# Kernel tuning notes

Measured on AMD Instinct MI355X. Metric: run time of the kernel, lower is better.

The kernel has to match this reference:

```python
import jax, jax.numpy as jnp
import numpy as np

DIM, HEADS, WS, SHIFT, HID = 256, 8, 7, 3, 1024
N = WS * WS

def _rel_index():
    coords = np.stack(np.meshgrid(np.arange(WS), np.arange(WS), indexing='ij')).reshape(2, -1)
    rel = (coords[:, :, None] - coords[:, None, :]).transpose(1, 2, 0)
    rel[:, :, 0] += WS - 1
    rel[:, :, 1] += WS - 1
    rel[:, :, 0] *= 2 * WS - 1
    return rel.sum(-1)  # [N, N] int

def _attn_mask(hp, wp):
    img = np.zeros((hp, wp))
    slices = (slice(0, -WS), slice(-WS, -SHIFT), slice(-SHIFT, None))
    cnt = 0
    for hs in slices:
        for ws_ in slices:
            img[hs, ws_] = cnt
            cnt += 1
    mw = img.reshape(hp // WS, WS, wp // WS, WS).transpose(0, 2, 1, 3).reshape(-1, N)
    am = mw[:, None, :] - mw[:, :, None]  # [nw, N, N]
    return np.where(am != 0, -100.0, 0.0).astype(np.float32)

def _ln(t, g, b):
    mu = t.mean(-1, keepdims=True)
    var = ((t - mu) ** 2).mean(-1, keepdims=True)
    return (t - mu) / jnp.sqrt(var + 1e-5) * g + b

def setup_inputs() -> dict:
    key = jax.random.key(0)
    ks = jax.random.split(key, 16)
    b, h, w = 16, 112, 112
    p = lambda k, shape: jax.random.normal(k, shape, dtype=jnp.float32) * 0.02
    return {
        'x': jax.random.normal(ks[0], (b, h * w, DIM), dtype=jnp.float32),
        'norm1_w': jnp.ones((DIM,), jnp.float32), 'norm1_b': jnp.zeros((DIM,), jnp.float32),
        'qkv_w': p(ks[1], (DIM, 3 * DIM)), 'qkv_b': jnp.zeros((3 * DIM,), jnp.float32),
        'proj_w': p(ks[2], (DIM, DIM)), 'proj_b': jnp.zeros((DIM,), jnp.float32),
        'bias_table': p(ks[3], ((2 * WS - 1) * (2 * WS - 1), HEADS)),
        'norm2_w': jnp.ones((DIM,), jnp.float32), 'norm2_b': jnp.zeros((DIM,), jnp.float32),
        'fc1_w': p(ks[4], (DIM, HID)), 'fc1_b': jnp.zeros((HID,), jnp.float32),
        'fc2_w': p(ks[5], (HID, DIM)), 'fc2_b': jnp.zeros((DIM,), jnp.float32),
        'h': h, 'w': w,
    }

def reference(x, norm1_w, norm1_b, qkv_w, qkv_b, proj_w, proj_b, bias_table,
              norm2_w, norm2_b, fc1_w, fc1_b, fc2_w, fc2_b, h, w):
    b, l, c = x.shape
    hd = c // HEADS
    shortcut = x
    xn = _ln(x, norm1_w, norm1_b).reshape(b, h, w, c)
    pad_b, pad_r = (-h) % WS, (-w) % WS
    if pad_b or pad_r:
        xn = jnp.pad(xn, ((0, 0), (0, pad_b), (0, pad_r), (0, 0)))
    hp, wp = h + pad_b, w + pad_r
    xs = jnp.roll(xn, (-SHIFT, -SHIFT), (1, 2))
    # window partition -> [B_, N, c]
    win = xs.reshape(b, hp // WS, WS, wp // WS, WS, c).transpose(0, 1, 3, 2, 4, 5).reshape(-1, N, c)
    qkv = (win @ qkv_w + qkv_b).reshape(-1, N, 3, HEADS, hd).transpose(2, 0, 3, 1, 4)
    q, k, v = qkv[0] * (hd ** -0.5), qkv[1], qkv[2]
    attn = jnp.einsum('bhnd,bhmd->bhnm', q, k)  # [B_, H, N, N]
    rpb = bias_table[jnp.asarray(_rel_index().reshape(-1))].reshape(N, N, HEADS).transpose(2, 0, 1)
    attn = attn + rpb[None]
    mask = jnp.asarray(_attn_mask(hp, wp))  # [nw, N, N]
    nw = mask.shape[0]
    attn = (attn.reshape(b, nw, HEADS, N, N) + mask[None, :, None]).reshape(-1, HEADS, N, N)
    attn = jax.nn.softmax(attn, axis=-1)
    out = jnp.einsum('bhnm,bhmd->bhnd', attn, v).transpose(0, 2, 1, 3).reshape(-1, N, c)
    out = out @ proj_w + proj_b
    # window reverse
    out = out.reshape(b, hp // WS, wp // WS, WS, WS, c).transpose(0, 1, 3, 2, 4, 5).reshape(b, hp, wp, c)
    out = jnp.roll(out, (SHIFT, SHIFT), (1, 2))[:, :h, :w].reshape(b, h * w, c)
    x = shortcut + out
    x = x + (jax.nn.gelu(_ln(x, norm2_w, norm2_b) @ fc1_w + fc1_b, approximate=False) @ fc2_w + fc2_b)
    return x
```

## Files before the change

kernel.cpp:

```cpp
#include <hip/hip_runtime.h>
#include <stdint.h>
#include <math.h>

#define DIMC   256
#define NHEADS 8
#define WSZ    7
#define NTOK   49
#define HIDN   1024
#define IMGS   112
#define BATCH  16
#define NWIN   4096
#define MTOT   200704

using frag_ab = __attribute__((ext_vector_type(8))) short;
using frag_cd = __attribute__((ext_vector_type(4))) float;

__device__ __forceinline__ float b2f(ushort u) {
    union { float f; uint32_t i; } c; c.i = ((uint32_t)u) << 16; return c.f;
}
__device__ __forceinline__ ushort f2b(float f) {
    union { float f; uint32_t i; } c; c.f = f;
    uint32_t r = c.i + 0x7fffu + ((c.i >> 16) & 1u);
    return (ushort)(r >> 16);
}

__device__ __forceinline__ void gld16(const ushort* g, ushort* l) {
    __builtin_amdgcn_global_load_lds(
        (const __attribute__((address_space(1))) void*)g,
        (__attribute__((address_space(3))) void*)l, 16, 0, 0);
}

__global__ void detect_kernel(const uint32_t* __restrict__ w, int* __restrict__ flag) {
    if (threadIdx.x == 0 && blockIdx.x == 0)
        *flag = (w[0] == 0x3F800000u) ? 1 : 0;
}

__global__ void cvt_kernel(const void* __restrict__ src, ushort* __restrict__ dst,
                           int n, const int* __restrict__ dflag) {
    int i = blockIdx.x * 256 + threadIdx.x;
    if (i < n)
        dst[i] = (*dflag) ? f2b(((const float*)src)[i]) : ((const ushort*)src)[i];
}

__global__ void transpose_cvt(const void* __restrict__ src, ushort* __restrict__ dst,
                              int K, int N, const int* __restrict__ dflag) {
    int idx = blockIdx.x * 256 + threadIdx.x;
    if (idx < K * N) {
        int k = idx / N, n = idx - k * N;
        ushort v = (*dflag) ? f2b(((const float*)src)[idx]) : ((const ushort*)src)[idx];
        dst[n * K + k] = v;
    }
}

__global__ __launch_bounds__(256)
void zero_vpad(ushort* __restrict__ vt) {
    int idx = blockIdx.x * 256 + threadIdx.x;
    float4 z = {0.f, 0.f, 0.f, 0.f};
    *(float4*)(vt + ((size_t)(idx >> 1) << 6) + 48 + (idx & 1) * 8) = z;
}

template <bool REMAP>
__global__ __launch_bounds__(256)
void ln_kernel(const void* __restrict__ xin, const ushort* __restrict__ g,
               const ushort* __restrict__ bt, ushort* __restrict__ out,
               const int* __restrict__ dflag) {
    int gw = (blockIdx.x * 256 + threadIdx.x) >> 6;
    int lane = threadIdx.x & 63;
    if (gw >= MTOT) return;
    float v0, v1, v2, v3;
    if constexpr (REMAP) {
        if (*dflag) {
            float4 xv = *(const float4*)((const float*)xin + (size_t)gw * DIMC + lane * 4);
            v0 = xv.x; v1 = xv.y; v2 = xv.z; v3 = xv.w;
        } else {
            ushort4 xv = *(const ushort4*)((const ushort*)xin + (size_t)gw * DIMC + lane * 4);
            v0 = b2f(xv.x); v1 = b2f(xv.y); v2 = b2f(xv.z); v3 = b2f(xv.w);
        }
    } else {
        ushort4 xv = *(const ushort4*)((const ushort*)xin + (size_t)gw * DIMC + lane * 4);
        v0 = b2f(xv.x); v1 = b2f(xv.y); v2 = b2f(xv.z); v3 = b2f(xv.w);
    }
    float s = v0 + v1 + v2 + v3;
#pragma unroll
    for (int off = 32; off; off >>= 1) s += __shfl_xor(s, off);
    float mean = s * (1.f / 256.f);
    float d0 = v0 - mean, d1 = v1 - mean, d2 = v2 - mean, d3 = v3 - mean;
    float q = d0 * d0 + d1 * d1 + d2 * d2 + d3 * d3;
#pragma unroll
    for (int off = 32; off; off >>= 1) q += __shfl_xor(q, off);
    float inv = rsqrtf(q * (1.f / 256.f) + 1e-5f);
    ushort4 gv = *(const ushort4*)(g + lane * 4);
    ushort4 bv = *(const ushort4*)(bt + lane * 4);
    ushort4 o;
    o.x = f2b(d0 * inv * b2f(gv.x) + b2f(bv.x));
    o.y = f2b(d1 * inv * b2f(gv.y) + b2f(bv.y));
    o.z = f2b(d2 * inv * b2f(gv.z) + b2f(bv.z));
    o.w = f2b(d3 * inv * b2f(gv.w) + b2f(bv.w));
    size_t orow;
    if constexpr (REMAP) {
        int b = gw / 12544, sres = gw - b * 12544;
        int row = sres / IMGS, col = sres - row * IMGS;
        int r = row - 3; if (r < 0) r += IMGS;
        int c = col - 3; if (c < 0) c += IMGS;
        int wh = r / WSZ, tr = r - wh * WSZ;
        int ww = c / WSZ, tc = c - ww * WSZ;
        orow = (size_t)(((b * 16 + wh) * 16 + ww)) * NTOK + (tr * WSZ + tc);
    } else {
        orow = gw;
    }
    *(ushort4*)(out + orow * DIMC + lane * 4) = o;
}

template <int MODE>
__global__ __launch_bounds__(256)
void gemm_bt(const ushort* __restrict__ A, const ushort* __restrict__ Bt,
             const ushort* __restrict__ bias, void* __restrict__ outv,
             const void* __restrict__ add, int M, int N, int K,
             const int* __restrict__ dflag) {
    __shared__ __align__(16) ushort As[2][128 * 32];
    __shared__ __align__(16) ushort Bs[2][128 * 32];
    const int t = threadIdx.x;
    const int lane = t & 63, wave = t >> 6;
    const int wr = (wave >> 1) * 64, wc = (wave & 1) * 64;
    const int lrow = lane & 15, lq8 = (lane >> 4) * 8;
    const int bm = blockIdx.y * 128, bn = blockIdx.x * 128;
    const int arow = t >> 2, acol = (t & 3) * 8;

    int isf32 = 0;
    if constexpr (MODE == 1) isf32 = *dflag;

    frag_cd acc[4][4];
#pragma unroll
    for (int i = 0; i < 4; i++)
#pragma unroll
        for (int j = 0; j < 4; j++) acc[i][j] = (frag_cd){0.f, 0.f, 0.f, 0.f};

    const ushort* Ag0 = A + (size_t)(bm + arow) * K + acol;
    const ushort* Ag1 = Ag0 + (size_t)64 * K;
    const ushort* Bg0 = Bt + (size_t)(bn + arow) * K + acol;
    const ushort* Bg1 = Bg0 + (size_t)64 * K;
    const int lofs0 = arow * 32 + acol;
    const int lofs1 = (arow + 64) * 32 + acol;

    gld16(Ag0, &As[0][lofs0]);
    gld16(Ag1, &As[0][lofs1]);
    gld16(Bg0, &Bs[0][lofs0]);
    gld16(Bg1, &Bs[0][lofs1]);
    __syncthreads();

    int cur = 0;
    for (int kk = 0; kk < K; kk += 32) {
        const int nxt = cur ^ 1;
        if (kk + 32 < K) {
            gld16(Ag0 + kk + 32, &As[nxt][lofs0]);
            gld16(Ag1 + kk + 32, &As[nxt][lofs1]);
            gld16(Bg0 + kk + 32, &Bs[nxt][lofs0]);
            gld16(Bg1 + kk + 32, &Bs[nxt][lofs1]);
        }
        frag_ab af[4], bfr[4];
#pragma unroll
        for (int i = 0; i < 4; i++)
            af[i] = *(const frag_ab*)&As[cur][(wr + i * 16 + lrow) * 32 + lq8];
#pragma unroll
        for (int j = 0; j < 4; j++)
            bfr[j] = *(const frag_ab*)&Bs[cur][(wc + j * 16 + lrow) * 32 + lq8];
#pragma unroll
        for (int i = 0; i < 4; i++)
#pragma unroll
            for (int j = 0; j < 4; j++)
                acc[i][j] = __builtin_amdgcn_mfma_f32_16x16x32_bf16(
                    af[i], bfr[j], acc[i][j], 0, 0, 0);
        __syncthreads();
        cur = nxt;
    }

    ushort* out = (ushort*)outv;
    float*  outf = (float*)outv;

#pragma unroll
    for (int i = 0; i < 4; i++) {
#pragma unroll
        for (int rg = 0; rg < 4; rg++) {
            const int gm = bm + wr + i * 16 + (lane >> 4) * 4 + rg;
            int win = 0, tok = 0;
            size_t rowbase = 0;
            if constexpr (MODE == 0) {
                win = gm / 49; tok = gm - win * 49;
            } else if constexpr (MODE == 1) {
                win = gm / 49; tok = gm - win * 49;
                int b = win >> 8, wh = (win >> 4) & 15, ww = win & 15;
                int tr = tok / 7, tc = tok - tr * 7;
                int r = wh * 7 + tr + 3; if (r >= IMGS) r -= IMGS;
                int c = ww * 7 + tc + 3; if (c >= IMGS) c -= IMGS;
                rowbase = ((size_t)b * 12544 + r * IMGS + c) * DIMC;
            } else {
                rowbase = (size_t)gm * N;
            }
#pragma unroll
            for (int j = 0; j < 4; j++) {
                const int gn = bn + wc + j * 16 + lrow;
                float v = acc[i][j][rg] + b2f(bias[gn]);
                if constexpr (MODE == 0) {
                    int part = gn >> 8, hd = (gn >> 5) & 7, dd = gn & 31;
                    if (part == 0) v *= 0.17677669529663687f;
                    if (part == 2) {
                        out[(size_t)2 * MTOT * DIMC +
                            (((size_t)win * NHEADS + hd) * 32 + dd) * 64 + tok] = f2b(v);
                    } else {
                        out[(size_t)part * ((size_t)MTOT * DIMC) +
                            (((size_t)win * NHEADS + hd) * NTOK + tok) * 32 + dd] = f2b(v);
                    }
                } else if constexpr (MODE == 1) {
                    float r = isf32 ? ((const float*)add)[rowbase + gn]
                                    : b2f(((const ushort*)add)[rowbase + gn]);
                    v += r;
                    out[rowbase + gn] = f2b(v);
                } else if constexpr (MODE == 2) {
                    v = 0.5f * v * (1.f + erff(v * 0.70710678118654752f));
                    out[rowbase + gn] = f2b(v);
                } else {
                    v += b2f(((const ushort*)add)[rowbase + gn]);
                    outf[rowbase + gn] = v;
                }
            }
        }
    }
}

__global__ __launch_bounds__(256)
void attn_kernel(const ushort* __restrict__ qb, const ushort* __restrict__ kb,
                 const ushort* __restrict__ vtb, const ushort* __restrict__ btab,
                 ushort* __restrict__ out) {
    __shared__ __align__(16) ushort Pl[4][2][16][72];
    __shared__ float bbs[4][172];
    const int t = threadIdx.x;
    const int wv = t >> 6, l = t & 63;
    const int lo = l & 15, hi = l >> 4;
    const int gw = blockIdx.x * 4 + wv;
    const int win = gw >> 3, hd = gw & 7;
    const int wh = (win >> 4) & 15, ww = win & 15;

    for (int idx = l; idx < 169; idx += 64)
        bbs[wv][idx] = b2f(btab[idx * NHEADS + hd]);

    const ushort* qp = qb  + (size_t)gw * (NTOK * 32);
    const ushort* kp = kb  + (size_t)gw * (NTOK * 32);
    const ushort* vp = vtb + (size_t)gw * (32 * 64);

    frag_ab af[4], bfr[4];
#pragma unroll
    for (int i = 0; i < 4; i++) {
        af[i]  = *(const frag_ab*)(qp + (i * 16 + lo) * 32 + hi * 8);
        bfr[i] = *(const frag_ab*)(kp + (i * 16 + lo) * 32 + hi * 8);
    }
    frag_ab vf[2][2];
#pragma unroll
    for (int j = 0; j < 2; j++)
#pragma unroll
        for (int kk = 0; kk < 2; kk++)
            vf[j][kk] = *(const frag_ab*)(vp + (j * 16 + lo) * 64 + kk * 32 + hi * 8);

    frag_cd S[4][4];
#pragma unroll
    for (int i = 0; i < 4; i++)
#pragma unroll
        for (int j = 0; j < 4; j++) S[i][j] = (frag_cd){0.f, 0.f, 0.f, 0.f};
#pragma unroll
    for (int i = 0; i < 4; i++)
#pragma unroll
        for (int j = 0; j < 4; j++)
            S[i][j] = __builtin_amdgcn_mfma_f32_16x16x32_bf16(af[i], bfr[j], S[i][j], 0, 0, 0);

    int cy[4], cx[4], rvj[4], rhj[4];
#pragma unroll
    for (int j = 0; j < 4; j++) {
        int c = j * 16 + lo;
        int y = (c * 9363) >> 16;
        cy[j] = y; cx[j] = c - y * 7;
        rvj[j] = (wh < 15) ? 0 : ((cy[j] < 4) ? 1 : 2);
        rhj[j] = (ww < 15) ? 0 : ((cx[j] < 4) ? 1 : 2);
    }

    frag_cd o[4][2];
#pragma unroll
    for (int i = 0; i < 4; i++)
#pragma unroll
        for (int j = 0; j < 2; j++) o[i][j] = (frag_cd){0.f, 0.f, 0.f, 0.f};

#pragma unroll
    for (int i = 0; i < 4; i++) {
        const int cur = i & 1;
#pragma unroll
        for (int rg = 0; rg < 4; rg++) {
            int r = i * 16 + hi * 4 + rg;
            int rr = (r < NTOK) ? r : 0;
            int yi = (rr * 9363) >> 16, xi = rr - yi * 7;
            int rvi = (wh < 15) ? 0 : ((yi < 4) ? 1 : 2);
            int rhi = (ww < 15) ? 0 : ((xi < 4) ? 1 : 2);
            float xs[4];
#pragma unroll
            for (int j = 0; j < 4; j++) {
                bool valid = (j < 3) | (lo == 0);
                float v = S[i][j][rg]
                        + bbs[wv][(yi - cy[j] + 6) * 13 + (xi - cx[j] + 6)];
                v = (rvi != rvj[j] || rhi != rhj[j]) ? v - 100.f : v;
                xs[j] = valid ? v : -1e30f;
            }
            float m = fmaxf(fmaxf(xs[0], xs[1]), fmaxf(xs[2], xs[3]));
#pragma unroll
            for (int off = 8; off; off >>= 1) m = fmaxf(m, __shfl_xor(m, off));
            float e0 = __expf(xs[0] - m);
            float e1 = __expf(xs[1] - m);
            float e2 = __expf(xs[2] - m);
            float e3 = __expf(xs[3] - m);
            float sum = e0 + e1 + e2 + e3;
#pragma unroll
            for (int off = 8; off; off >>= 1) sum += __shfl_xor(sum, off);
            float inv = 1.f / sum;
            int rl = hi * 4 + rg;
            int sw = ((rl >> 3) & 1) << 4;
            ushort* prow = &Pl[wv][cur][rl][0];
            prow[(lo +  0) ^ sw] = f2b(e0 * inv);
            prow[(lo + 16) ^ sw] = f2b(e1 * inv);
            prow[(lo + 32) ^ sw] = f2b(e2 * inv);
            prow[(lo + 48) ^ sw] = f2b(e3 * inv);
        }
        int swr = ((lo >> 3) & 1) << 4;
        frag_ab pa0 = *(const frag_ab*)&Pl[wv][cur][lo][(      hi * 8) ^ swr];
        frag_ab pa1 = *(const frag_ab*)&Pl[wv][cur][lo][(32 + hi * 8) ^ swr];
#pragma unroll
        for (int j = 0; j < 2; j++) {
            o[i][j] = __builtin_amdgcn_mfma_f32_16x16x32_bf16(pa0, vf[j][0], o[i][j], 0, 0, 0);
            o[i][j] = __builtin_amdgcn_mfma_f32_16x16x32_bf16(pa1, vf[j][1], o[i][j], 0, 0, 0);
        }
    }

#pragma unroll
    for (int i = 0; i < 4; i++)
#pragma unroll
        for (int rg = 0; rg < 4; rg++) {
            int r = i * 16 + hi * 4 + rg;
            if (r < NTOK) {
                size_t ob = ((size_t)win * NTOK + r) * DIMC + hd * 32;
                out[ob + lo]      = f2b(o[i][0][rg]);
                out[ob + 16 + lo] = f2b(o[i][1][rg]);
            }
        }
}

extern "C" void kernel_launch(void* const* d_in, const int* in_sizes, int n_in,
                              void* d_out, int out_size, void* d_ws, size_t ws_size,
                              hipStream_t stream) {
    (void)in_sizes; (void)n_in; (void)out_size;
    const void* x        = d_in[0];
    const void* norm1_w  = d_in[1];
    const void* norm1_b  = d_in[2];
    const void* qkv_w    = d_in[3];
    const void* qkv_b    = d_in[4];
    const void* proj_w   = d_in[5];
    const void* proj_b   = d_in[6];
    const void* btab     = d_in[7];
    const void* norm2_w  = d_in[8];
    const void* norm2_b  = d_in[9];
    const void* fc1_w    = d_in[10];
    const void* fc1_b    = d_in[11];
    const void* fc2_w    = d_in[12];
    const void* fc2_b    = d_in[13];

    const size_t szA   = (size_t)MTOT * DIMC * 2;
    const size_t szBIG = (size_t)MTOT * HIDN * 2;
    const size_t szWT  = (size_t)(768 * 256 + 256 * 256 + 256 * 1024 + 1024 * 256) * 2;
    const size_t szSV  = 16384;
    const size_t need  = szSV + szA * 2 + szBIG + szWT;
    if (ws_size < need) return;

    char* ws = (char*)d_ws;
    ushort* sv    = (ushort*)ws;
    ushort* svN1w = sv + 0;
    ushort* svN1b = sv + 256;
    ushort* svQKb = sv + 512;
    ushort* svPJb = sv + 1280;
    ushort* svN2w = sv + 1536;
    ushort* svN2b = sv + 1792;
    ushort* svF1b = sv + 2048;
    ushort* svF2b = sv + 3072;
    ushort* svBT  = sv + 3328;
    int*    dflag = (int*)(ws + szSV - 256);

    char* big = ws + szSV;
    ushort* bufA   = (ushort*)big;
    ushort* bufBIG = (ushort*)(big + szA);
    ushort* bufQ   = bufBIG;
    ushort* bufK   = bufBIG + (size_t)MTOT * DIMC;
    ushort* bufV   = bufBIG + (size_t)2 * MTOT * DIMC;
    ushort* bufX1  = (ushort*)(big + szA + szBIG);
    ushort* qkvT   = (ushort*)(big + szA + szBIG + szA);
    ushort* projT  = qkvT + 768 * 256;
    ushort* fc1T   = projT + 256 * 256;
    ushort* fc2T   = fc1T + 256 * 1024;

    detect_kernel<<<1, 64, 0, stream>>>((const uint32_t*)norm1_w, dflag);

    zero_vpad<<<8192, 256, 0, stream>>>(bufV);

    cvt_kernel<<<1, 256, 0, stream>>>(norm1_w, svN1w, 256, dflag);
    cvt_kernel<<<1, 256, 0, stream>>>(norm1_b, svN1b, 256, dflag);
    cvt_kernel<<<3, 256, 0, stream>>>(qkv_b,  svQKb, 768, dflag);
    cvt_kernel<<<1, 256, 0, stream>>>(proj_b, svPJb, 256, dflag);
    cvt_kernel<<<1, 256, 0, stream>>>(norm2_w, svN2w, 256, dflag);
    cvt_kernel<<<1, 256, 0, stream>>>(norm2_b, svN2b, 256, dflag);
    cvt_kernel<<<4, 256, 0, stream>>>(fc1_b,  svF1b, 1024, dflag);
    cvt_kernel<<<1, 256, 0, stream>>>(fc2_b,  svF2b, 256, dflag);
    cvt_kernel<<<6, 256, 0, stream>>>(btab,   svBT, 1352, dflag);

    transpose_cvt<<<(768 * 256 + 255) / 256, 256, 0, stream>>>(qkv_w, qkvT, 256, 768, dflag);
    transpose_cvt<<<(256 * 256 + 255) / 256, 256, 0, stream>>>(proj_w, projT, 256, 256, dflag);
    transpose_cvt<<<(256 * 1024 + 255) / 256, 256, 0, stream>>>(fc1_w, fc1T, 256, 1024, dflag);
    transpose_cvt<<<(1024 * 256 + 255) / 256, 256, 0, stream>>>(fc2_w, fc2T, 1024, 256, dflag);

    ln_kernel<true><<<MTOT / 4, 256, 0, stream>>>(x, svN1w, svN1b, bufA, dflag);

    gemm_bt<0><<<dim3(768 / 128, MTOT / 128), 256, 0, stream>>>(
        bufA, qkvT, svQKb, bufBIG, nullptr, MTOT, 768, 256, dflag);

    attn_kernel<<<NWIN * NHEADS / 4, 256, 0, stream>>>(bufQ, bufK, bufV, svBT, bufA);

    gemm_bt<1><<<dim3(256 / 128, MTOT / 128), 256, 0, stream>>>(
        bufA, projT, svPJb, bufX1, x, MTOT, 256, 256, dflag);

    ln_kernel<false><<<MTOT / 4, 256, 0, stream>>>(bufX1, svN2w, svN2b, bufA, dflag);

    gemm_bt<2><<<dim3(1024 / 128, MTOT / 128), 256, 0, stream>>>(
        bufA, fc1T, svF1b, bufBIG, nullptr, MTOT, 1024, 256, dflag);

    gemm_bt<3><<<dim3(256 / 128, MTOT / 128), 256, 0, stream>>>(
        bufBIG, fc2T, svF2b, d_out, bufX1, MTOT, 256, 1024, dflag);
}
```

Measured before the change: 1.561 ms.

## Swizzle GEMM blocks per XCD and transpose V in LDS inside attention

GEMM launches become 1D grids, with block indices remapped so each of the 8 XCDs handles a contiguous range of M tiles. This should improve L2 reuse of A rows across the N tiles. The QKV GEMM now writes V in the same token-major layout as Q and K instead of a padded transposed layout, so the zero_vpad pre-pass goes away. The attention kernel instead loads V rows and transposes them through a new LDS buffer, which adds LDS traffic and registers per wave.

```diff
diff --git a/kernel.cpp b/kernel.cpp
--- a/kernel.cpp
+++ b/kernel.cpp
@@ -50,13 +50,6 @@
         ushort v = (*dflag) ? f2b(((const float*)src)[idx]) : ((const ushort*)src)[idx];
         dst[n * K + k] = v;
     }
-}
-
-__global__ __launch_bounds__(256)
-void zero_vpad(ushort* __restrict__ vt) {
-    int idx = blockIdx.x * 256 + threadIdx.x;
-    float4 z = {0.f, 0.f, 0.f, 0.f};
-    *(float4*)(vt + ((size_t)(idx >> 1) << 6) + 48 + (idx & 1) * 8) = z;
 }
 
 template <bool REMAP>
@@ -116,14 +109,18 @@
 void gemm_bt(const ushort* __restrict__ A, const ushort* __restrict__ Bt,
              const ushort* __restrict__ bias, void* __restrict__ outv,
              const void* __restrict__ add, int M, int N, int K,
-             const int* __restrict__ dflag) {
+             const int* __restrict__ dflag, int nbn) {
     __shared__ __align__(16) ushort As[2][128 * 32];
     __shared__ __align__(16) ushort Bs[2][128 * 32];
     const int t = threadIdx.x;
     const int lane = t & 63, wave = t >> 6;
     const int wr = (wave >> 1) * 64, wc = (wave & 1) * 64;
     const int lrow = lane & 15, lq8 = (lane >> 4) * 8;
-    const int bm = blockIdx.y * 128, bn = blockIdx.x * 128;
+    const int lid = blockIdx.x;
+    const int xcd = lid & 7, idx = lid >> 3;
+    const int ppx = (M >> 7) >> 3;
+    const int bn = (idx % nbn) * 128;
+    const int bm = (xcd * ppx + idx / nbn) * 128;
     const int arow = t >> 2, acol = (t & 3) * 8;
 
     int isf32 = 0;
@@ -203,13 +200,8 @@
                 if constexpr (MODE == 0) {
                     int part = gn >> 8, hd = (gn >> 5) & 7, dd = gn & 31;
                     if (part == 0) v *= 0.17677669529663687f;
-                    if (part == 2) {
-                        out[(size_t)2 * MTOT * DIMC +
-                            (((size_t)win * NHEADS + hd) * 32 + dd) * 64 + tok] = f2b(v);
-                    } else {
-                        out[(size_t)part * ((size_t)MTOT * DIMC) +
-                            (((size_t)win * NHEADS + hd) * NTOK + tok) * 32 + dd] = f2b(v);
-                    }
+                    out[(size_t)part * ((size_t)MTOT * DIMC) +
+                        (((size_t)win * NHEADS + hd) * NTOK + tok) * 32 + dd] = f2b(v);
                 } else if constexpr (MODE == 1) {
                     float r = isf32 ? ((const float*)add)[rowbase + gn]
                                     : b2f(((const ushort*)add)[rowbase + gn]);
@@ -229,9 +221,10 @@
 
 __global__ __launch_bounds__(256)
 void attn_kernel(const ushort* __restrict__ qb, const ushort* __restrict__ kb,
-                 const ushort* __restrict__ vtb, const ushort* __restrict__ btab,
+                 const ushort* __restrict__ vb, const ushort* __restrict__ btab,
                  ushort* __restrict__ out) {
     __shared__ __align__(16) ushort Pl[4][2][16][72];
+    __shared__ __align__(16) ushort Vl[4][32][72];
     __shared__ float bbs[4][172];
     const int t = threadIdx.x;
     const int wv = t >> 6, l = t & 63;
@@ -243,9 +236,18 @@
     for (int idx = l; idx < 169; idx += 64)
         bbs[wv][idx] = b2f(btab[idx * NHEADS + hd]);
 
-    const ushort* qp = qb  + (size_t)gw * (NTOK * 32);
-    const ushort* kp = kb  + (size_t)gw * (NTOK * 32);
-    const ushort* vp = vtb + (size_t)gw * (32 * 64);
+    const ushort* qp = qb + (size_t)gw * (NTOK * 32);
+    const ushort* kp = kb + (size_t)gw * (NTOK * 32);
+    const ushort* vp = vb + (size_t)gw * (NTOK * 32);
+
+    frag_ab vreg[4];
+#pragma unroll
+    for (int q = 0; q < 4; q++) {
+        if (l < NTOK)
+            vreg[q] = *(const frag_ab*)(vp + l * 32 + q * 8);
+        else
+            vreg[q] = (frag_ab){0, 0, 0, 0, 0, 0, 0, 0};
+    }
 
     frag_ab af[4], bfr[4];
 #pragma unroll
@@ -253,13 +255,6 @@
         af[i]  = *(const frag_ab*)(qp + (i * 16 + lo) * 32 + hi * 8);
         bfr[i] = *(const frag_ab*)(kp + (i * 16 + lo) * 32 + hi * 8);
     }
-    frag_ab vf[2][2];
-#pragma unroll
-    for (int j = 0; j < 2; j++)
-#pragma unroll
-        for (int kk = 0; kk < 2; kk++)
-            vf[j][kk] = *(const frag_ab*)(vp + (j * 16 + lo) * 64 + kk * 32 + hi * 8);
-
     frag_cd S[4][4];
 #pragma unroll
     for (int i = 0; i < 4; i++)
@@ -270,6 +265,18 @@
 #pragma unroll
         for (int j = 0; j < 4; j++)
             S[i][j] = __builtin_amdgcn_mfma_f32_16x16x32_bf16(af[i], bfr[j], S[i][j], 0, 0, 0);
+
+#pragma unroll
+    for (int q = 0; q < 4; q++)
+#pragma unroll
+        for (int e = 0; e < 8; e++)
+            Vl[wv][q * 8 + e][l] = (ushort)vreg[q][e];
+    frag_ab vf[2][2];
+#pragma unroll
+    for (int j = 0; j < 2; j++)
+#pragma unroll
+        for (int kk = 0; kk < 2; kk++)
+            vf[j][kk] = *(const frag_ab*)&Vl[wv][j * 16 + lo][kk * 32 + hi * 8];
 
     int cy[4], cx[4], rvj[4], rhj[4];
 #pragma unroll
@@ -401,8 +408,6 @@
 
     detect_kernel<<<1, 64, 0, stream>>>((const uint32_t*)norm1_w, dflag);
 
-    zero_vpad<<<8192, 256, 0, stream>>>(bufV);
-
     cvt_kernel<<<1, 256, 0, stream>>>(norm1_w, svN1w, 256, dflag);
     cvt_kernel<<<1, 256, 0, stream>>>(norm1_b, svN1b, 256, dflag);
     cvt_kernel<<<3, 256, 0, stream>>>(qkv_b,  svQKb, 768, dflag);
@@ -420,19 +425,19 @@
 
     ln_kernel<true><<<MTOT / 4, 256, 0, stream>>>(x, svN1w, svN1b, bufA, dflag);
 
-    gemm_bt<0><<<dim3(768 / 128, MTOT / 128), 256, 0, stream>>>(
-        bufA, qkvT, svQKb, bufBIG, nullptr, MTOT, 768, 256, dflag);
+    gemm_bt<0><<<6 * (MTOT / 128), 256, 0, stream>>>(
+        bufA, qkvT, svQKb, bufBIG, nullptr, MTOT, 768, 256, dflag, 6);
 
     attn_kernel<<<NWIN * NHEADS / 4, 256, 0, stream>>>(bufQ, bufK, bufV, svBT, bufA);
 
-    gemm_bt<1><<<dim3(256 / 128, MTOT / 128), 256, 0, stream>>>(
-        bufA, projT, svPJb, bufX1, x, MTOT, 256, 256, dflag);
+    gemm_bt<1><<<2 * (MTOT / 128), 256, 0, stream>>>(
+        bufA, projT, svPJb, bufX1, x, MTOT, 256, 256, dflag, 2);
 
     ln_kernel<false><<<MTOT / 4, 256, 0, stream>>>(bufX1, svN2w, svN2b, bufA, dflag);
 
-    gemm_bt<2><<<dim3(1024 / 128, MTOT / 128), 256, 0, stream>>>(
-        bufA, fc1T, svF1b, bufBIG, nullptr, MTOT, 1024, 256, dflag);
-
-    gemm_bt<3><<<dim3(256 / 128, MTOT / 128), 256, 0, stream>>>(
-        bufBIG, fc2T, svF2b, d_out, bufX1, MTOT, 256, 1024, dflag);
-}
+    gemm_bt<2><<<8 * (MTOT / 128), 256, 0, stream>>>(
+        bufA, fc1T, svF1b, bufBIG, nullptr, MTOT, 1024, 256, dflag, 8);
+
+    gemm_bt<3><<<2 * (MTOT / 128), 256, 0, stream>>>(
+        bufBIG, fc2T, svF2b, d_out, bufX1, MTOT, 256, 1024, dflag, 2);
+}
```

Measured after the change: 1.462 ms. 6.3% less time.
